# Kernel optimization log

Measured on AMD Instinct MI355X. Metric: run time of the kernel, lower is better.

## Reference

```python
import jax, jax.numpy as jnp
import numpy as np

B = 32768
D_IN = 512      # input_dim == dict_dim (forced by the STE add)
HID = 512       # hard-coded hidden width of linear1
D = 512         # dict_dim / embedding_dim
P = 8           # per_factor_dict_size: number of codebooks / MLP branches
K = 10          # num_factor: codebook size (rows per embedding table)
COMMIT = 0.25


def setup_inputs() -> dict:
    key = jax.random.key(0)
    ks = jax.random.split(key, 7)
    s1 = 1.0 / np.sqrt(D_IN)
    s2 = 1.0 / np.sqrt(HID)
    return {
        "inputs": jax.random.normal(ks[0], (B, D_IN), jnp.float32),
        "W1": jax.random.uniform(ks[1], (P, HID, D_IN), jnp.float32, -s1, s1),
        "b1": jax.random.uniform(ks[2], (P, HID), jnp.float32, -s1, s1),
        "W2": jax.random.uniform(ks[3], (P, D, HID), jnp.float32, -s2, s2),
        "b2": jax.random.uniform(ks[4], (P, D), jnp.float32, -s2, s2),
        # embedding init: uniform(-1/num_factor, 1/num_factor)
        "E": jax.random.uniform(ks[5], (P, K, D), jnp.float32, -1.0 / K, 1.0 / K),
        "label_gen": jax.random.randint(ks[6], (B,), 0, K, jnp.int64),
    }


def reference(inputs, W1, b1, W2, b2, E, label_gen):
    sg = jax.lax.stop_gradient
    # P parallel 2-layer MLPs: [P, B, D]
    h = jax.nn.relu(jnp.einsum("bd,phd->pbh", inputs, W1) + b1[:, None, :])
    z = jnp.einsum("pbh,peh->pbe", h, W2) + b2[:, None, :]
    # squared-distance expansion per codebook: [P, B, K]
    distances = (
        jnp.sum(z * z, axis=-1, keepdims=True)
        + jnp.sum(E * E, axis=-1)[:, None, :]
        - 2.0 * jnp.einsum("pbd,pkd->pbk", z, E)
    )
    ave_distances = jnp.mean(distances, axis=0)          # [B, K]
    idx = jnp.argmin(ave_distances, axis=1)              # [B]
    # one-hot @ E[p] then mean over p == mean codebook gathered at idx
    Emean = jnp.mean(E, axis=0)                          # [K, D]
    vq = Emean[idx]                                      # [B, D]
    vq_z = inputs + sg(vq - inputs)                      # straight-through
    # all_vq_z[j] = mean_p E[p, j]; losses vs every code row: [K, B]
    diff1 = Emean[:, None, :] - sg(inputs)[None, :, :]   # [K, B, D]
    diff2 = sg(Emean)[:, None, :] - inputs[None, :, :]
    all_vq_loss = jnp.sum(diff1 * diff1, axis=-1) + COMMIT * jnp.sum(diff2 * diff2, axis=-1)
    all_vq_z = inputs[None, :, :] + sg(Emean[:, None, :] - inputs[None, :, :])  # [K, B, D]
    changed_vq_z = Emean[label_gen]                      # [B, D]
    return (vq_z, distances, all_vq_z, all_vq_loss, changed_vq_z)
```

## Files before the change

kernel.cpp:

```cpp
#include <hip/hip_runtime.h>
#include <stdint.h>

typedef _Float16 f16;
typedef _Float16 f16x4 __attribute__((ext_vector_type(4)));
typedef _Float16 f16x8 __attribute__((ext_vector_type(8)));
typedef float f32x4 __attribute__((ext_vector_type(4)));

#define B_ROWS 32768
#define DIM 512
#define NP 8
#define NK 10

typedef __attribute__((address_space(3))) unsigned int lds_u32;
typedef __attribute__((address_space(1))) const unsigned int gbl_u32;

__device__ __forceinline__ void gload_lds16(const void* g, void* l) {
  __builtin_amdgcn_global_load_lds((gbl_u32*)(uintptr_t)g, (lds_u32*)(uintptr_t)l, 16, 0, 0);
}


__global__ void prep_split(const float4* __restrict__ X4, f16x4* __restrict__ Xh4,
                           f16x4* __restrict__ Xl4, const float4* __restrict__ W14,
                           f16x4* __restrict__ W1h4, f16x4* __restrict__ W1l4,
                           const float4* __restrict__ W24, f16x4* __restrict__ W2h4) {
  int bid = blockIdx.x, tid = threadIdx.x;
  if (bid < 1024) {
    for (int i = bid * 256 + tid; i < 4194304; i += 1024 * 256) {
      float4 v = X4[i];
      f16x4 h = {(f16)v.x, (f16)v.y, (f16)v.z, (f16)v.w};
      f16x4 l = {(f16)(v.x - (float)h[0]), (f16)(v.y - (float)h[1]),
                 (f16)(v.z - (float)h[2]), (f16)(v.w - (float)h[3])};
      Xh4[i] = h;
      Xl4[i] = l;
    }
  } else if (bid < 1152) {
    for (int i = (bid - 1024) * 256 + tid; i < 524288; i += 128 * 256) {
      float4 v = W14[i];
      f16x4 h = {(f16)v.x, (f16)v.y, (f16)v.z, (f16)v.w};
      f16x4 l = {(f16)(v.x - (float)h[0]), (f16)(v.y - (float)h[1]),
                 (f16)(v.z - (float)h[2]), (f16)(v.w - (float)h[3])};
      W1h4[i] = h;
      W1l4[i] = l;
    }
  } else {
    for (int i = (bid - 1152) * 256 + tid; i < 524288; i += 128 * 256) {
      float4 v = W24[i];
      f16x4 h = {(f16)v.x, (f16)v.y, (f16)v.z, (f16)v.w};
      W2h4[i] = h;
    }
  }
}


__global__ void enorm2(const float* __restrict__ E, float* __restrict__ Emean,
                       float* __restrict__ E2, float* __restrict__ E2m) {
  int bid = blockIdx.x;
  int lane = threadIdx.x;
  if (bid < 80) {
    const float* src = E + (size_t)bid * DIM;
    float s = 0.f;
    for (int i = lane; i < DIM; i += 64) {
      float v = src[i];
      s = fmaf(v, v, s);
    }
#pragma unroll
    for (int m = 1; m < 64; m <<= 1) s += __shfl_xor(s, m, 64);
    if (lane == 0) E2[bid] = s;
  } else {
    int k = bid - 80;
    float acc = 0.f;
    for (int i = lane; i < DIM; i += 64) {
      float s = 0.f;
#pragma unroll
      for (int p = 0; p < NP; ++p) s += E[p * NK * DIM + k * DIM + i];
      s *= 0.125f;
      Emean[k * DIM + i] = s;
      acc = fmaf(s, s, acc);
    }
#pragma unroll
    for (int m = 1; m < 64; m <<= 1) acc += __shfl_xor(acc, m, 64);
    if (lane == 0) E2m[k] = acc;
  }
}


__global__ __launch_bounds__(512) void etilde_kernel(const float* __restrict__ W2,
                                                     const float* __restrict__ b2,
                                                     const float* __restrict__ E,
                                                     f16* __restrict__ EimgH,
                                                     f16* __restrict__ EimgL,
                                                     float* __restrict__ c_) {
  const int p = blockIdx.x / NK, k = blockIdx.x % NK;
  const int h = threadIdx.x;
  __shared__ float Er[512];
  __shared__ float red[8];
  Er[h] = E[((size_t)p * NK + k) * DIM + h];
  __syncthreads();
  const float* Wp = W2 + (size_t)p * DIM * DIM;
  float s = 0.f;
#pragma unroll 8
  for (int d = 0; d < DIM; ++d) s = fmaf(Wp[(size_t)d * DIM + h], Er[d], s);
  int ei = p * 8320 + k * 520 + h;
  f16 hi = (f16)s;
  EimgH[ei] = hi;
  EimgL[ei] = (f16)(s - (float)hi);
  if (h < 8) {
    int pi = p * 8320 + k * 520 + 512 + h;
    EimgH[pi] = (f16)0.f;
    EimgL[pi] = (f16)0.f;
  }
  if (k == 0) {
    for (int j = h; j < 6 * 520; j += 512) {
      int pi = p * 8320 + 10 * 520 + j;
      EimgH[pi] = (f16)0.f;
      EimgL[pi] = (f16)0.f;
    }
  }
  float t = b2[p * DIM + h] * Er[h];
#pragma unroll
  for (int m = 1; m < 64; m <<= 1) t += __shfl_xor(t, m, 64);
  if ((h & 63) == 0) red[h >> 6] = t;
  __syncthreads();
  if (h == 0) {
    float cc = 0.f;
#pragma unroll
    for (int i = 0; i < 8; ++i) cc += red[i];
    c_[p * NK + k] = cc;
  }
}


template <int EPI, int NBN, int NPROD, int GRP>
__global__ __launch_bounds__(256) void gemmA(
    const f16* __restrict__ Ah_, const f16* __restrict__ Al_, int lda, int apitch,
    const f16* __restrict__ Bh_, const f16* __restrict__ Bl_, int bpitch,
    const float* __restrict__ bias_, int bias_pitch,
    f16* __restrict__ Oh, f16* __restrict__ Ol, int ldo,
    float* __restrict__ part2) {
  __shared__ f16 smem[32768];
  const int tid = threadIdx.x;
  const int lane = tid & 63;
  const int wave = tid >> 6;
  const int wr = wave >> 1, wc = wave & 1;
  const int p = blockIdx.z;

  const int q8 = gridDim.x >> 3;
  const int bid = blockIdx.x;
  const int swz = (bid & 7) * q8 + (bid >> 3);
  const int band = swz / (GRP * NBN);
  const int r_ = swz % (GRP * NBN);
  const int bm = band * GRP + (r_ % GRP);
  const int bn = r_ / GRP;
  const int m0 = bm * 128, n0 = bn * 128;

  const f16* Ahp = Ah_ + (size_t)p * apitch;
  const f16* Alp = Al_ + (size_t)p * apitch;
  const f16* Bhp = Bh_ + (size_t)p * bpitch;
  const f16* Blp = Bl_ + (size_t)p * bpitch;

  const int NT = (NPROD == 3) ? 24 : 8;

  f32x4 acc[4][4] = {};

  auto stage = [&](int buf, int t) {
    const f16* As;
    const f16* Bs;
    int k0;
    if (NPROD == 3) {
      int pr = t % 3;
      As = (pr == 2) ? Alp : Ahp;
      Bs = (pr == 1) ? Blp : Bhp;
      k0 = (t / 3) * 64;
    } else {
      As = Ahp;
      Bs = Bhp;
      k0 = t * 64;
    }
    f16* sA = smem + buf * 16384;
    f16* sB = sA + 8192;
#pragma unroll
    for (int j = 0; j < 4; ++j) {
      int r = j * 32 + (tid >> 3);
      int c = ((tid & 7) ^ (r & 7)) * 8;
      gload_lds16(As + (size_t)(m0 + r) * lda + k0 + c, sA + j * 2048 + tid * 8);
      gload_lds16(Bs + (size_t)(n0 + r) * 512 + k0 + c, sB + j * 2048 + tid * 8);
    }
  };

  stage(0, 0);
  __syncthreads();

  const int g = lane >> 4, rl = lane & 15;

  for (int s = 0; s < NT; ++s) {
    int nx = s + 1;
    if (nx < NT) stage(nx & 1, nx);
    const char* sA = (const char*)(smem + (s & 1) * 16384);
    const char* sB = sA + 16384;
    f16x8 af[4][2], bf[4][2];
#pragma unroll
    for (int i = 0; i < 4; ++i) {
      int ra = wr * 64 + i * 16 + rl;
      int rb = wc * 64 + i * 16 + rl;
#pragma unroll
      for (int kk = 0; kk < 2; ++kk) {
        int cb = kk * 64 + g * 16;
        af[i][kk] = *(const f16x8*)(sA + ra * 128 + (cb ^ ((ra & 7) << 4)));
        bf[i][kk] = *(const f16x8*)(sB + rb * 128 + (cb ^ ((rb & 7) << 4)));
      }
    }
#pragma unroll
    for (int i = 0; i < 4; ++i)
#pragma unroll
      for (int jn = 0; jn < 4; ++jn)
#pragma unroll
        for (int kk = 0; kk < 2; ++kk)
          acc[i][jn] = __builtin_amdgcn_mfma_f32_16x16x32_f16(af[i][kk], bf[jn][kk], acc[i][jn], 0, 0, 0);
    __syncthreads();
  }

  if (EPI == 0) {
#pragma unroll
    for (int jn = 0; jn < 4; ++jn) {
      int cg = n0 + wc * 64 + jn * 16 + rl;
      float bv = bias_[cg];
#pragma unroll
      for (int i = 0; i < 4; ++i) {
        int r0 = m0 + wr * 64 + i * 16 + g * 4;
#pragma unroll
        for (int r = 0; r < 4; ++r) {
          float z = acc[i][jn][r] + bv;
          z = fmaxf(z, 0.f);
          f16 h = (f16)z;
          size_t off = (size_t)(r0 + r) * ldo + cg;
          Oh[off] = h;
          Ol[off] = (f16)(z - (float)h);
        }
      }
    }
  } else {
    const float* bp = bias_ + (size_t)p * bias_pitch;
    float bvals[4];
#pragma unroll
    for (int jn = 0; jn < 4; ++jn) bvals[jn] = bp[n0 + wc * 64 + jn * 16 + rl];
    const int ch = bn * 2 + wc;
    float* pb = part2 + (size_t)(p * 8 + ch) * B_ROWS;
#pragma unroll
    for (int i = 0; i < 4; ++i) {
#pragma unroll
      for (int r = 0; r < 4; ++r) {
        float q = 0.f;
#pragma unroll
        for (int jn = 0; jn < 4; ++jn) {
          float z = acc[i][jn][r] + bvals[jn];
          q = fmaf(z, z, q);
        }
#pragma unroll
        for (int m = 1; m < 16; m <<= 1) q += __shfl_xor(q, m, 64);
        if (rl == 0) pb[m0 + wr * 64 + i * 16 + g * 4 + r] = q;
      }
    }
  }
}


__global__ __launch_bounds__(256) void dots_mfma(const f16* __restrict__ Hh,
                                                 const f16* __restrict__ Hl,
                                                 const f16* __restrict__ EimgH,
                                                 const f16* __restrict__ EimgL,
                                                 const float* __restrict__ c_,
                                                 float* __restrict__ gout) {
  __shared__ f16 sH[2][4096];
  __shared__ f16 sL[2][4096];
  __shared__ f16 sEh[16 * 520];
  __shared__ f16 sEl[16 * 520];
  const int tid = threadIdx.x;
  const int lane = tid & 63, wave = tid >> 6;
  const int p = blockIdx.y;
  const int r0 = blockIdx.x * 64;
  {
    const uint32_t* ih = (const uint32_t*)(EimgH + (size_t)p * 16 * 520);
    const uint32_t* il = (const uint32_t*)(EimgL + (size_t)p * 16 * 520);
    uint32_t* oh = (uint32_t*)sEh;
    uint32_t* ol = (uint32_t*)sEl;
    for (int i = tid; i < 16 * 520 / 2; i += 256) {
      oh[i] = ih[i];
      ol[i] = il[i];
    }
  }
  const int gq = lane >> 4, rl = lane & 15;

  auto stageT = [&](int buf, int t) {
#pragma unroll
    for (int rnd = 0; rnd < 2; ++rnd) {
      int w = rnd * 256 + tid;
      int r = w >> 3;
      int c = ((w & 7) ^ (r & 7)) * 8;
      gload_lds16(Hh + (size_t)(r0 + r) * 4096 + p * DIM + t * 64 + c, &sH[buf][(size_t)w * 8]);
      gload_lds16(Hl + (size_t)(r0 + r) * 4096 + p * DIM + t * 64 + c, &sL[buf][(size_t)w * 8]);
    }
  };

  f32x4 acc = {};
  stageT(0, 0);
  __syncthreads();

  for (int t = 0; t < 8; ++t) {
    if (t < 7) stageT((t + 1) & 1, t + 1);
    const char* bh = (const char*)sH[t & 1];
    const char* bl = (const char*)sL[t & 1];
    const int ra = wave * 16 + rl;
    f16x8 ah[2], al[2], beh[2], bel[2];
#pragma unroll
    for (int kk = 0; kk < 2; ++kk) {
      int cb = kk * 64 + gq * 16;
      ah[kk] = *(const f16x8*)(bh + ra * 128 + (cb ^ ((ra & 7) << 4)));
      al[kk] = *(const f16x8*)(bl + ra * 128 + (cb ^ ((ra & 7) << 4)));
      int ce = t * 128 + kk * 64 + gq * 16;
      beh[kk] = *(const f16x8*)((const char*)sEh + rl * 1040 + ce);
      bel[kk] = *(const f16x8*)((const char*)sEl + rl * 1040 + ce);
    }
#pragma unroll
    for (int kk = 0; kk < 2; ++kk) {
      acc = __builtin_amdgcn_mfma_f32_16x16x32_f16(ah[kk], beh[kk], acc, 0, 0, 0);
      acc = __builtin_amdgcn_mfma_f32_16x16x32_f16(ah[kk], bel[kk], acc, 0, 0, 0);
      acc = __builtin_amdgcn_mfma_f32_16x16x32_f16(al[kk], beh[kk], acc, 0, 0, 0);
    }
    __syncthreads();
  }
  if (rl < NK) {
    float cv = c_[p * NK + rl];
#pragma unroll
    for (int r = 0; r < 4; ++r) {
      int row = r0 + wave * 16 + gq * 4 + r;
      gout[((size_t)p * B_ROWS + row) * NK + rl] = acc[r] + cv;
    }
  }
}


__global__ __launch_bounds__(256) void final_kernel(
    const float* __restrict__ X, const float* __restrict__ part2,
    float* __restrict__ gdist, const float* __restrict__ E2,
    const float* __restrict__ Emean, const float* __restrict__ E2m,
    const int* __restrict__ label, float* __restrict__ vq_z,
    float* __restrict__ avz, float* __restrict__ loss, float* __restrict__ changed) {
  __shared__ float Em[NK * DIM];
  __shared__ float e2s[NK];
  const int tid = threadIdx.x;
  for (int i = tid; i < NK * DIM; i += 256) Em[i] = Emean[i];
  if (tid < NK) e2s[tid] = E2m[tid];
  __syncthreads();

  const int b0 = blockIdx.x * 16;
  {
    const float4* Em4 = (const float4*)Em;
    float4* avz4 = (float4*)avz;
    if (blockIdx.x < 256) {
      for (int it = 0; it < 80; ++it) {
        int idx = it * 256 + tid;
        int d4 = idx & 127, row = (idx >> 7) & 15, k = idx >> 11;
        if (k == 8) continue;
        avz4[(((size_t)k * B_ROWS + b0 + row) << 7) + d4] = Em4[k * 128 + d4];
      }
    } else {
      for (int it = 0; it < 80; ++it) {
        int idx = it * 256 + tid;
        int d4 = idx & 127, row = (idx >> 7) & 15, k = idx >> 11;
        avz4[(((size_t)k * B_ROWS + b0 + row) << 7) + d4] = Em4[k * 128 + d4];
      }
    }
  }

  const int lane = tid & 63, wave = tid >> 6;
  const int pl = lane & 7, kh = lane >> 3;
  for (int rr = 0; rr < 4; ++rr) {
    int b = b0 + wave * 4 + rr;
    float zq = part2[(size_t)(pl * 8 + kh) * B_ROWS + b];
    zq += __shfl_xor(zq, 8, 64);
    zq += __shfl_xor(zq, 16, 64);
    zq += __shfl_xor(zq, 32, 64);
    float g0 = gdist[((size_t)pl * B_ROWS + b) * NK + kh];
    float g1 = (lane < 16) ? gdist[((size_t)pl * B_ROWS + b) * NK + 8 + kh] : 0.f;
    float dv0 = zq + E2[pl * NK + kh] - 2.f * g0;
    float dv1 = zq + E2[pl * NK + 8 + kh] - 2.f * g1;
    gdist[((size_t)pl * B_ROWS + b) * NK + kh] = dv0;
    if (lane < 16) gdist[((size_t)pl * B_ROWS + b) * NK + 8 + kh] = dv1;
    float v0 = dv0, v1 = (lane < 16) ? dv1 : 0.f;
#pragma unroll
    for (int m = 1; m < 8; m <<= 1) {
      v0 += __shfl_xor(v0, m, 64);
      v1 += __shfl_xor(v1, m, 64);
    }
    float a[NK];
#pragma unroll
    for (int k = 0; k < 8; ++k) a[k] = __shfl(v0, k * 8, 64);
    a[8] = __shfl(v1, 0, 64);
    a[9] = __shfl(v1, 8, 64);
    int idx = 0;
    float mn = a[0];
#pragma unroll
    for (int k = 1; k < NK; ++k) {
      if (a[k] < mn) { mn = a[k]; idx = k; }
    }
    const float* xr = X + (size_t)b * DIM;
    float sx = 0.f, dx[NK] = {};
#pragma unroll
    for (int j = 0; j < 8; ++j) {
      float x = xr[j * 64 + lane];
      sx = fmaf(x, x, sx);
#pragma unroll
      for (int k = 0; k < NK; ++k) dx[k] = fmaf(x, Em[k * DIM + j * 64 + lane], dx[k]);
    }
#pragma unroll
    for (int m = 1; m < 64; m <<= 1) {
      sx += __shfl_xor(sx, m, 64);
#pragma unroll
      for (int k = 0; k < NK; ++k) dx[k] += __shfl_xor(dx[k], m, 64);
    }
    if (lane == 0) {
#pragma unroll
      for (int k = 0; k < NK; ++k)
        loss[(size_t)k * B_ROWS + b] = 1.25f * (sx - 2.f * dx[k] + e2s[k]);
    }
    int lab = label[b];
#pragma unroll
    for (int j = 0; j < 8; ++j) {
      int c = j * 64 + lane;
      vq_z[(size_t)b * DIM + c] = Em[idx * DIM + c];
      changed[(size_t)b * DIM + c] = Em[lab * DIM + c];
    }
  }
}


__global__ void bcast_rest(const float* __restrict__ Emean, float4* __restrict__ avz4) {
  const float4* Em4 = (const float4*)Emean;
  int tid = blockIdx.x * 256 + threadIdx.x;
  for (int it = 0; it < 32; ++it) {
    int idx = tid + it * 16384;
    int b = idx >> 7, d4 = idx & 127;
    avz4[((size_t)(8 * B_ROWS + b) << 7) + d4] = Em4[8 * 128 + d4];
  }
}


extern "C" void kernel_launch(void* const* d_in, const int* in_sizes, int n_in,
                              void* d_out, int out_size, void* d_ws, size_t ws_size,
                              hipStream_t stream) {
  const float* X = (const float*)d_in[0];
  const float* W1 = (const float*)d_in[1];
  const float* b1 = (const float*)d_in[2];
  const float* W2 = (const float*)d_in[3];
  const float* b2 = (const float*)d_in[4];
  const float* E = (const float*)d_in[5];
  const int* lab = (const int*)d_in[6];
  float* out = (float*)d_out;

  float* vq_z = out;
  float* dist = out + 16777216;
  float* avz = out + 16777216 + 2621440;
  float* loss = avz + 167772160;
  float* chg = loss + 327680;

  f16* Xh = (f16*)vq_z;
  f16* Xl = Xh + 16777216;
  f16* Hh = (f16*)avz;
  f16* Hl = Hh + 134217728;
  float* part2 = avz + 134217728;

  char* w = (char*)d_ws;
  f16* W1h = (f16*)w; w += 4194304;
  f16* W1l = (f16*)w; w += 4194304;
  f16* W2h = (f16*)w; w += 4194304;
  float* Emean = (float*)w; w += NK * DIM * 4;
  float* E2 = (float*)w; w += 512;
  float* E2m = (float*)w; w += 256;
  float* c_ = (float*)w; w += 512;
  f16* EimgH = (f16*)w; w += NP * 16 * 520 * 2;
  f16* EimgL = (f16*)w; w += NP * 16 * 520 * 2;

  prep_split<<<1280, 256, 0, stream>>>((const float4*)X, (f16x4*)Xh, (f16x4*)Xl,
                                       (const float4*)W1, (f16x4*)W1h, (f16x4*)W1l,
                                       (const float4*)W2, (f16x4*)W2h);
  enorm2<<<90, 64, 0, stream>>>(E, Emean, E2, E2m);
  etilde_kernel<<<80, 512, 0, stream>>>(W2, b2, E, EimgH, EimgL, c_);

  gemmA<0, 32, 3, 8><<<dim3(8192, 1, 1), 256, 0, stream>>>(
      Xh, Xl, 512, 0, W1h, W1l, 0, b1, 0, Hh, Hl, 4096, nullptr);
  gemmA<1, 4, 1, 1><<<dim3(1024, 1, NP), 256, 0, stream>>>(
      Hh, Hh, 4096, 512, W2h, W2h, 262144, b2, 512, nullptr, nullptr, 0, part2);

  dots_mfma<<<dim3(512, NP), 256, 0, stream>>>(Hh, Hl, EimgH, EimgL, c_, dist);
  final_kernel<<<2048, 256, 0, stream>>>(X, part2, dist, E2, Emean, E2m, lab,
                                         vq_z, avz, loss, chg);
  bcast_rest<<<64, 256, 0, stream>>>(Emean, (float4*)avz);
}
```

Measured before the change: 1.110 ms.

## Merge second-layer GEMM and codebook dot kernels into one launch

Combines the second MLP layer GEMM (which yields the squared norms of z) and the codebook dot-product kernel into a single launch. Blocks are partitioned by blockIdx.x, and both share one LDS pool. The two independent workloads can now run concurrently and fill the GPU better, and one launch boundary goes away. The cost is that every block reserves the larger LDS footprint (about 64KB), which can lower occupancy for the lighter dot-product blocks.

```diff
diff --git a/kernel.cpp b/kernel.cpp
--- a/kernel.cpp
+++ b/kernel.cpp
@@ -264,76 +264,158 @@
 }
 
 
-__global__ __launch_bounds__(256) void dots_mfma(const f16* __restrict__ Hh,
-                                                 const f16* __restrict__ Hl,
-                                                 const f16* __restrict__ EimgH,
-                                                 const f16* __restrict__ EimgL,
-                                                 const float* __restrict__ c_,
-                                                 float* __restrict__ gout) {
-  __shared__ f16 sH[2][4096];
-  __shared__ f16 sL[2][4096];
-  __shared__ f16 sEh[16 * 520];
-  __shared__ f16 sEl[16 * 520];
+__global__ __launch_bounds__(256) void g2d_union(
+    const f16* __restrict__ Hh, const f16* __restrict__ Hl,
+    const f16* __restrict__ W2h, const float* __restrict__ b2,
+    const f16* __restrict__ EimgH, const f16* __restrict__ EimgL,
+    const float* __restrict__ c_, float* __restrict__ part2,
+    float* __restrict__ gout) {
+  __shared__ char pool[66048];
   const int tid = threadIdx.x;
-  const int lane = tid & 63, wave = tid >> 6;
   const int p = blockIdx.y;
-  const int r0 = blockIdx.x * 64;
-  {
-    const uint32_t* ih = (const uint32_t*)(EimgH + (size_t)p * 16 * 520);
-    const uint32_t* il = (const uint32_t*)(EimgL + (size_t)p * 16 * 520);
-    uint32_t* oh = (uint32_t*)sEh;
-    uint32_t* ol = (uint32_t*)sEl;
-    for (int i = tid; i < 16 * 520 / 2; i += 256) {
-      oh[i] = ih[i];
-      ol[i] = il[i];
-    }
-  }
-  const int gq = lane >> 4, rl = lane & 15;
-
-  auto stageT = [&](int buf, int t) {
-#pragma unroll
-    for (int rnd = 0; rnd < 2; ++rnd) {
-      int w = rnd * 256 + tid;
-      int r = w >> 3;
-      int c = ((w & 7) ^ (r & 7)) * 8;
-      gload_lds16(Hh + (size_t)(r0 + r) * 4096 + p * DIM + t * 64 + c, &sH[buf][(size_t)w * 8]);
-      gload_lds16(Hl + (size_t)(r0 + r) * 4096 + p * DIM + t * 64 + c, &sL[buf][(size_t)w * 8]);
-    }
-  };
-
-  f32x4 acc = {};
-  stageT(0, 0);
-  __syncthreads();
-
-  for (int t = 0; t < 8; ++t) {
-    if (t < 7) stageT((t + 1) & 1, t + 1);
-    const char* bh = (const char*)sH[t & 1];
-    const char* bl = (const char*)sL[t & 1];
-    const int ra = wave * 16 + rl;
-    f16x8 ah[2], al[2], beh[2], bel[2];
-#pragma unroll
-    for (int kk = 0; kk < 2; ++kk) {
-      int cb = kk * 64 + gq * 16;
-      ah[kk] = *(const f16x8*)(bh + ra * 128 + (cb ^ ((ra & 7) << 4)));
-      al[kk] = *(const f16x8*)(bl + ra * 128 + (cb ^ ((ra & 7) << 4)));
-      int ce = t * 128 + kk * 64 + gq * 16;
-      beh[kk] = *(const f16x8*)((const char*)sEh + rl * 1040 + ce);
-      bel[kk] = *(const f16x8*)((const char*)sEl + rl * 1040 + ce);
-    }
-#pragma unroll
-    for (int kk = 0; kk < 2; ++kk) {
-      acc = __builtin_amdgcn_mfma_f32_16x16x32_f16(ah[kk], beh[kk], acc, 0, 0, 0);
-      acc = __builtin_amdgcn_mfma_f32_16x16x32_f16(ah[kk], bel[kk], acc, 0, 0, 0);
-      acc = __builtin_amdgcn_mfma_f32_16x16x32_f16(al[kk], beh[kk], acc, 0, 0, 0);
-    }
+
+  if (blockIdx.x < 1024) {
+    f16* smem = (f16*)pool;
+    const int lane = tid & 63, wave = tid >> 6;
+    const int wr = wave >> 1, wc = wave & 1;
+    const int bid = blockIdx.x;
+    const int swz = (bid & 7) * 128 + (bid >> 3);
+    const int bm = swz >> 2, bn = swz & 3;
+    const int m0 = bm * 128, n0 = bn * 128;
+    const f16* Ahp = Hh + (size_t)p * 512;
+    const f16* Bhp = W2h + (size_t)p * 262144;
+
+    f32x4 acc[4][4] = {};
+
+    auto stage = [&](int buf, int t) {
+      int k0 = t * 64;
+      f16* sA = smem + buf * 16384;
+      f16* sB = sA + 8192;
+#pragma unroll
+      for (int j = 0; j < 4; ++j) {
+        int r = j * 32 + (tid >> 3);
+        int c = ((tid & 7) ^ (r & 7)) * 8;
+        gload_lds16(Ahp + (size_t)(m0 + r) * 4096 + k0 + c, sA + j * 2048 + tid * 8);
+        gload_lds16(Bhp + (size_t)(n0 + r) * 512 + k0 + c, sB + j * 2048 + tid * 8);
+      }
+    };
+
+    stage(0, 0);
     __syncthreads();
-  }
-  if (rl < NK) {
-    float cv = c_[p * NK + rl];
-#pragma unroll
-    for (int r = 0; r < 4; ++r) {
-      int row = r0 + wave * 16 + gq * 4 + r;
-      gout[((size_t)p * B_ROWS + row) * NK + rl] = acc[r] + cv;
+    const int g = lane >> 4, rl = lane & 15;
+    for (int s = 0; s < 8; ++s) {
+      if (s + 1 < 8) stage((s + 1) & 1, s + 1);
+      const char* sA = (const char*)(smem + (s & 1) * 16384);
+      const char* sB = sA + 16384;
+      f16x8 af[4][2], bf[4][2];
+#pragma unroll
+      for (int i = 0; i < 4; ++i) {
+        int ra = wr * 64 + i * 16 + rl;
+        int rb = wc * 64 + i * 16 + rl;
+#pragma unroll
+        for (int kk = 0; kk < 2; ++kk) {
+          int cb = kk * 64 + g * 16;
+          af[i][kk] = *(const f16x8*)(sA + ra * 128 + (cb ^ ((ra & 7) << 4)));
+          bf[i][kk] = *(const f16x8*)(sB + rb * 128 + (cb ^ ((rb & 7) << 4)));
+        }
+      }
+#pragma unroll
+      for (int i = 0; i < 4; ++i)
+#pragma unroll
+        for (int jn = 0; jn < 4; ++jn)
+#pragma unroll
+          for (int kk = 0; kk < 2; ++kk)
+            acc[i][jn] = __builtin_amdgcn_mfma_f32_16x16x32_f16(af[i][kk], bf[jn][kk], acc[i][jn], 0, 0, 0);
+      __syncthreads();
+    }
+
+    const float* bp = b2 + (size_t)p * 512;
+    float bvals[4];
+#pragma unroll
+    for (int jn = 0; jn < 4; ++jn) bvals[jn] = bp[n0 + wc * 64 + jn * 16 + rl];
+    const int ch = bn * 2 + wc;
+    float* pb = part2 + (size_t)(p * 8 + ch) * B_ROWS;
+#pragma unroll
+    for (int i = 0; i < 4; ++i) {
+#pragma unroll
+      for (int r = 0; r < 4; ++r) {
+        float q = 0.f;
+#pragma unroll
+        for (int jn = 0; jn < 4; ++jn) {
+          float z = acc[i][jn][r] + bvals[jn];
+          q = fmaf(z, z, q);
+        }
+#pragma unroll
+        for (int m = 1; m < 16; m <<= 1) q += __shfl_xor(q, m, 64);
+        if (rl == 0) pb[m0 + wr * 64 + i * 16 + g * 4 + r] = q;
+      }
+    }
+  } else {
+    f16* sH = (f16*)pool;
+    f16* sL = (f16*)(pool + 16384);
+    f16* sEh = (f16*)(pool + 32768);
+    f16* sEl = (f16*)(pool + 49408);
+    const int lane = tid & 63, wave = tid >> 6;
+    const int r0 = (blockIdx.x - 1024) * 64;
+    {
+      const uint32_t* ih = (const uint32_t*)(EimgH + (size_t)p * 16 * 520);
+      const uint32_t* il = (const uint32_t*)(EimgL + (size_t)p * 16 * 520);
+      uint32_t* oh = (uint32_t*)sEh;
+      uint32_t* ol = (uint32_t*)sEl;
+      for (int i = tid; i < 16 * 520 / 2; i += 256) {
+        oh[i] = ih[i];
+        ol[i] = il[i];
+      }
+    }
+    const int gq = lane >> 4, rl = lane & 15;
+
+    auto stageT = [&](int buf, int t) {
+#pragma unroll
+      for (int rnd = 0; rnd < 2; ++rnd) {
+        int w = rnd * 256 + tid;
+        int r = w >> 3;
+        int c = ((w & 7) ^ (r & 7)) * 8;
+        gload_lds16(Hh + (size_t)(r0 + r) * 4096 + p * DIM + t * 64 + c,
+                    sH + buf * 4096 + (size_t)w * 8);
+        gload_lds16(Hl + (size_t)(r0 + r) * 4096 + p * DIM + t * 64 + c,
+                    sL + buf * 4096 + (size_t)w * 8);
+      }
+    };
+
+    f32x4 acc = {};
+    stageT(0, 0);
+    __syncthreads();
+
+    for (int t = 0; t < 8; ++t) {
+      if (t < 7) stageT((t + 1) & 1, t + 1);
+      const char* bh = (const char*)(sH + (t & 1) * 4096);
+      const char* bl = (const char*)(sL + (t & 1) * 4096);
+      const int ra = wave * 16 + rl;
+      f16x8 ah[2], al[2], beh[2], bel[2];
+#pragma unroll
+      for (int kk = 0; kk < 2; ++kk) {
+        int cb = kk * 64 + gq * 16;
+        ah[kk] = *(const f16x8*)(bh + ra * 128 + (cb ^ ((ra & 7) << 4)));
+        al[kk] = *(const f16x8*)(bl + ra * 128 + (cb ^ ((ra & 7) << 4)));
+        int ce = t * 128 + kk * 64 + gq * 16;
+        beh[kk] = *(const f16x8*)((const char*)sEh + rl * 1040 + ce);
+        bel[kk] = *(const f16x8*)((const char*)sEl + rl * 1040 + ce);
+      }
+#pragma unroll
+      for (int kk = 0; kk < 2; ++kk) {
+        acc = __builtin_amdgcn_mfma_f32_16x16x32_f16(ah[kk], beh[kk], acc, 0, 0, 0);
+        acc = __builtin_amdgcn_mfma_f32_16x16x32_f16(ah[kk], bel[kk], acc, 0, 0, 0);
+        acc = __builtin_amdgcn_mfma_f32_16x16x32_f16(al[kk], beh[kk], acc, 0, 0, 0);
+      }
+      __syncthreads();
+    }
+    if (rl < NK) {
+      float cv = c_[p * NK + rl];
+#pragma unroll
+      for (int r = 0; r < 4; ++r) {
+        int row = r0 + wave * 16 + gq * 4 + r;
+        gout[((size_t)p * B_ROWS + row) * NK + rl] = acc[r] + cv;
+      }
     }
   }
 }
@@ -488,10 +570,10 @@
 
   gemmA<0, 32, 3, 8><<<dim3(8192, 1, 1), 256, 0, stream>>>(
       Xh, Xl, 512, 0, W1h, W1l, 0, b1, 0, Hh, Hl, 4096, nullptr);
-  gemmA<1, 4, 1, 1><<<dim3(1024, 1, NP), 256, 0, stream>>>(
-      Hh, Hh, 4096, 512, W2h, W2h, 262144, b2, 512, nullptr, nullptr, 0, part2);
-
-  dots_mfma<<<dim3(512, NP), 256, 0, stream>>>(Hh, Hl, EimgH, EimgL, c_, dist);
+
+  g2d_union<<<dim3(1536, NP), 256, 0, stream>>>(Hh, Hl, W2h, b2, EimgH, EimgL, c_,
+                                                part2, dist);
+
   final_kernel<<<2048, 256, 0, stream>>>(X, part2, dist, E2, Emean, E2m, lab,
                                          vq_z, avz, loss, chg);
   bcast_rest<<<64, 256, 0, stream>>>(Emean, (float4*)avz);
```

New measurement: 1.065 ms. -4.0%, faster.
